# Kernel tuning notes

Hardware: AMD Instinct MI355X
Metric: run time of the kernel (lower is better)

## Reference

```python
import jax, jax.numpy as jnp
import numpy as np

K_INIT = 16  # self.k from __init__

def setup_inputs() -> dict:
    key = jax.random.key(0)
    center = jax.random.normal(key, (8192, 64), dtype=jnp.float32)
    return {"center": center}

def _cdist(x):
    # Euclidean pairwise distances, matmul-based like torch.cdist(p=2).
    x2 = jnp.sum(x * x, axis=-1)  # [N]
    d2 = x2[:, None] + x2[None, :] - 2.0 * (x @ x.T)  # [N, N]
    d2 = jnp.maximum(d2, 0.0)
    # safe sqrt (grad-safe at 0; forward identical)
    d = jnp.sqrt(jnp.where(d2 > 0.0, d2, 1.0))
    return jnp.where(d2 > 0.0, d, 0.0)

def reference(center):
    n, d_feat = center.shape
    k = min(K_INIT + 1, d_feat)  # faithful to torch: min(self.k + 1, center.shape[1])
    dist = _cdist(center)  # [N, N]
    # smallest-k via top_k on negated distances
    _, indices = jax.lax.top_k(-dist, k)  # [N, k]
    neighbor_indices = indices[:, 1:]  # drop self, [N, k-1]
    mean_dists = jnp.take_along_axis(dist, neighbor_indices, axis=1).mean(axis=1)  # [N]
    logp = jax.nn.log_softmax(mean_dists, axis=0)  # = softmax(mean_dists).log()
    q = 1.0 / n
    # F.kl_div(p.log(), q, reduction='sum') = sum q * (log q - log p)
    loss = jnp.sum(q * (jnp.log(jnp.float32(q)) - logp))
    return loss
```

## Files before the change

### kernel.cpp

```cpp
#include <hip/hip_runtime.h>
#include <hip/hip_bf16.h>
#include <math.h>

#define N_PTS 8192
#define D_FEAT 64
#define TPB 1024
#define ROWS_B 32
#define PASSES 16
#define RSTR 648
#define LSTR 20

typedef __attribute__((ext_vector_type(8))) short short8v;
typedef __attribute__((ext_vector_type(16))) float f32x16;

__device__ ushort g_X2[N_PTS * D_FEAT];
__device__ float  g_x2n[N_PTS];
__device__ float  g_md[N_PTS];

__global__ __launch_bounds__(256) void pack_kernel(const float* __restrict__ x) {
    const int gt = blockIdx.x * 256 + threadIdx.x;
    const int row = gt >> 1, half = gt & 1;
    const int chunk = row >> 5, r = row & 31;
    const float4* xr = (const float4*)(x + (size_t)row * D_FEAT + half * 32);
    ushort* base = g_X2 + (size_t)chunk * 2048 + r * 8;
    float norm = 0.f;
    #pragma unroll
    for (int it = 0; it < 4; ++it) {
        float4 a = xr[2 * it], b = xr[2 * it + 1];
        float vals[8] = {a.x, a.y, a.z, a.w, b.x, b.y, b.z, b.w};
        uint hi[8];
        #pragma unroll
        for (int e = 0; e < 8; ++e) {
            float v = vals[e];
            norm += v * v;
            uint u = __float_as_uint(v);
            hi[e] = (u + 0x7fffu + ((u >> 16) & 1u)) >> 16;
        }
        *(uint4*)(base + (half * 4 + it) * 256) = make_uint4(
            hi[0] | (hi[1] << 16), hi[2] | (hi[3] << 16),
            hi[4] | (hi[5] << 16), hi[6] | (hi[7] << 16));
    }
    norm += __shfl_xor(norm, 1);
    if (half == 0) g_x2n[row] = norm;
}

#define CE(A, B) { float lo_, hi_; \
    asm("v_min_f32 %0, %2, %3\n\tv_max_f32 %1, %2, %3" \
        : "=&v"(lo_), "=&v"(hi_) : "v"(A), "v"(B)); \
    A = lo_; B = hi_; }
#define VMIN(D, A, B) { float r_; \
    asm("v_min_f32 %0, %1, %2" : "=v"(r_) : "v"(A), "v"(B)); D = r_; }

__global__ __launch_bounds__(TPB, 4) void nn_kernel() {
    __shared__ float s_mem[32 * RSTR];
    const int t    = threadIdx.x;
    const int lane = t & 63;
    const int w    = t >> 6;
    const int il   = lane & 31;
    const int h    = lane >> 5;
    const int ib   = blockIdx.x;
    const int i0   = ib * ROWS_B;
    const float INF = __builtin_inff();

    {
        float4* s4 = (float4*)s_mem;
        const float4* g4 = (const float4*)g_x2n;
        #pragma unroll
        for (int q = 0; q < 2; ++q) s4[t + q * TPB] = g4[t + q * TPB];
    }

    const short8v* Xf = (const short8v*)g_X2;

    short8v bfr[4];
    {
        const short8v* bp = Xf + ((size_t)ib * 8 + h) * 32 + il;
        #pragma unroll
        for (int tt = 0; tt < 4; ++tt) bfr[tt] = bp[tt * 64];
    }
    __syncthreads();

    float t16[16];
    #pragma unroll
    for (int k = 0; k < 16; ++k) t16[k] = INF;

    const short8v* abase = Xf + ((size_t)w * 8 + h) * 32 + il;
    #define ALOAD(dst, p) { \
        const short8v* ab_ = abase + (size_t)(p) * 4096; \
        _Pragma("unroll") \
        for (int tt = 0; tt < 4; ++tt) dst[tt] = ab_[tt * 64]; }

    #define EPILOG(accv, p) { \
        const int cl_ = (p) * 16 + w; \
        float c[16]; \
        _Pragma("unroll") \
        for (int g = 0; g < 4; ++g) { \
            float4 xq = *(const float4*)&s_mem[cl_ * 32 + 8 * g + 4 * h]; \
            float cand[4] = {xq.x, xq.y, xq.z, xq.w}; \
            _Pragma("unroll") \
            for (int e = 0; e < 4; ++e) \
                c[4 * g + e] = fmaf(-2.f, accv[4 * g + e], cand[e]); \
        } \
         \
        CE(c[0],c[8]) CE(c[1],c[9]) CE(c[2],c[10]) CE(c[3],c[11]) \
        CE(c[4],c[12]) CE(c[5],c[13]) CE(c[6],c[14]) CE(c[7],c[15]) \
        CE(c[0],c[4]) CE(c[1],c[5]) CE(c[2],c[6]) CE(c[3],c[7]) \
        CE(c[8],c[12]) CE(c[9],c[13]) CE(c[10],c[14]) CE(c[11],c[15]) \
        CE(c[4],c[8]) CE(c[5],c[9]) CE(c[6],c[10]) CE(c[7],c[11]) \
        CE(c[0],c[2]) CE(c[1],c[3]) CE(c[4],c[6]) CE(c[5],c[7]) \
        CE(c[8],c[10]) CE(c[9],c[11]) CE(c[12],c[14]) CE(c[13],c[15]) \
        CE(c[2],c[8]) CE(c[3],c[9]) CE(c[6],c[12]) CE(c[7],c[13]) \
        CE(c[2],c[4]) CE(c[3],c[5]) CE(c[6],c[8]) CE(c[7],c[9]) \
        CE(c[10],c[12]) CE(c[11],c[13]) \
        CE(c[0],c[1]) CE(c[2],c[3]) CE(c[4],c[5]) CE(c[6],c[7]) \
        CE(c[8],c[9]) CE(c[10],c[11]) CE(c[12],c[13]) CE(c[14],c[15]) \
        CE(c[1],c[8]) CE(c[3],c[10]) CE(c[5],c[12]) CE(c[7],c[14]) \
        CE(c[1],c[4]) CE(c[3],c[6]) CE(c[5],c[8]) CE(c[7],c[10]) \
        CE(c[9],c[12]) CE(c[11],c[14]) \
        CE(c[1],c[2]) CE(c[3],c[4]) CE(c[5],c[6]) CE(c[7],c[8]) \
        CE(c[9],c[10]) CE(c[11],c[12]) CE(c[13],c[14]) \
         \
        _Pragma("unroll") \
        for (int i = 0; i < 16; ++i) VMIN(t16[i], t16[i], c[15 - i]) \
        _Pragma("unroll") \
        for (int j = 8; j > 0; j >>= 1) { \
            _Pragma("unroll") \
            for (int i = 0; i < 16; ++i) { \
                const int ix = i ^ j; \
                if (ix > i) { CE(t16[i], t16[ix]) } \
            } \
        } }

    #define MFMA4(accv, areg) { \
        _Pragma("unroll") \
        for (int r = 0; r < 16; ++r) accv[r] = 0.f; \
        _Pragma("unroll") \
        for (int tt = 0; tt < 4; ++tt) \
            accv = __builtin_amdgcn_mfma_f32_32x32x16_bf16(areg[tt], bfr[tt], accv, 0, 0, 0); }

    short8v a0[4], a1[4];
    f32x16 acc;
    ALOAD(a0, 0);
    #pragma unroll 1
    for (int pp = 0; pp < PASSES / 2; ++pp) {
        const int p0 = 2 * pp, p1 = 2 * pp + 1;
        ALOAD(a1, p1);
        MFMA4(acc, a0);
        EPILOG(acc, p0);
        if (pp < PASSES / 2 - 1) ALOAD(a0, p0 + 2);
        MFMA4(acc, a1);
        EPILOG(acc, p1);
    }

    {
        const bool own = (w == (ib & 15)) && (h == ((il >> 2) & 1));
        if (own) {
            #pragma unroll
            for (int k = 0; k < 15; ++k) t16[k] = t16[k + 1];
            t16[15] = INF;
        }
    }

    __syncthreads();
    {
        const int list = w * 2 + h;
        float* dst = &s_mem[il * RSTR + list * LSTR];
        *(float4*)(dst + 0)  = make_float4(t16[0],  t16[1],  t16[2],  t16[3]);
        *(float4*)(dst + 4)  = make_float4(t16[4],  t16[5],  t16[6],  t16[7]);
        *(float4*)(dst + 8)  = make_float4(t16[8],  t16[9],  t16[10], t16[11]);
        *(float4*)(dst + 12) = make_float4(t16[12], t16[13], t16[14], t16[15]);
    }
    __syncthreads();

    {
        const int q  = lane >> 5;
        const int sl = lane & 31;
        const int r  = w * 2 + q;
        const int row = i0 + r;
        float tl[16];
        {
            const float* src = &s_mem[r * RSTR + sl * LSTR];
            float4 q0 = *(const float4*)(src + 0);
            float4 q1 = *(const float4*)(src + 4);
            float4 q2 = *(const float4*)(src + 8);
            float4 q3 = *(const float4*)(src + 12);
            tl[0]=q0.x; tl[1]=q0.y; tl[2]=q0.z; tl[3]=q0.w;
            tl[4]=q1.x; tl[5]=q1.y; tl[6]=q1.z; tl[7]=q1.w;
            tl[8]=q2.x; tl[9]=q2.y; tl[10]=q2.z; tl[11]=q2.w;
            tl[12]=q3.x; tl[13]=q3.y; tl[14]=q3.z; tl[15]=q3.w;
        }
        const float x2r = g_x2n[row];
        float sum = 0.f;
        #pragma unroll 1
        for (int it = 0; it < 16; ++it) {
            float m = tl[0]; int src = sl;
            #pragma unroll
            for (int off = 16; off > 0; off >>= 1) {
                float om = __shfl_xor(m, off);
                int os = __shfl_xor(src, off);
                if (om < m || (om == m && os < src)) { m = om; src = os; }
            }
            sum += sqrtf(fmaxf(m + x2r, 0.f));
            const bool pop = (sl == src);
            #pragma unroll
            for (int k = 0; k < 15; ++k) tl[k] = pop ? tl[k + 1] : tl[k];
            tl[15] = pop ? INF : tl[15];
        }
        if (sl == 0) g_md[row] = sum * (1.f / 16.f);
    }
}

__global__ __launch_bounds__(1024) void loss_kernel(float* __restrict__ out) {
    __shared__ float s[1024];
    const int t = threadIdx.x;

    float m = -__builtin_inff();
    for (int j = t; j < N_PTS; j += 1024) m = fmaxf(m, g_md[j]);
    s[t] = m; __syncthreads();
    for (int off = 512; off > 0; off >>= 1) {
        if (t < off) s[t] = fmaxf(s[t], s[t + off]);
        __syncthreads();
    }
    m = s[0]; __syncthreads();

    float se = 0.f, sm = 0.f;
    for (int j = t; j < N_PTS; j += 1024) {
        float v = g_md[j];
        se += expf(v - m);
        sm += v;
    }
    s[t] = se; __syncthreads();
    for (int off = 512; off > 0; off >>= 1) {
        if (t < off) s[t] += s[t + off];
        __syncthreads();
    }
    float S = s[0]; __syncthreads();
    s[t] = sm; __syncthreads();
    for (int off = 512; off > 0; off >>= 1) {
        if (t < off) s[t] += s[t + off];
        __syncthreads();
    }
    float M = s[0];

    if (t == 0) {
        const float n = (float)N_PTS;
        out[0] = -logf(n) - M / n + (m + logf(S));
    }
}

extern "C" void kernel_launch(void* const* d_in, const int* in_sizes, int n_in,
                              void* d_out, int out_size, void* d_ws, size_t ws_size,
                              hipStream_t stream) {
    const float* x = (const float*)d_in[0];
    float* out = (float*)d_out;

    pack_kernel<<<N_PTS * 2 / 256, 256, 0, stream>>>(x);
    nn_kernel<<<N_PTS / ROWS_B, TPB, 0, stream>>>();
    loss_kernel<<<1, 1024, 0, stream>>>(out);
}
```

Measured before the change: 57.99 us.

## Split candidate range across two blocks per row tile and merge partial top-16

Each 32-row tile is now processed by two 512-thread blocks, each scanning half of the candidate points. Each block writes its sorted top-16 partial distances to a global buffer. A new merge kernel combines the two lists per row, then takes sqrt and the mean. This doubles the grid and halves the block size to raise occupancy and parallelism, at the cost of an extra kernel launch and a global round trip for the partial lists.

```diff
diff --git a/kernel.cpp b/kernel.cpp
--- a/kernel.cpp
+++ b/kernel.cpp
@@ -4,17 +4,20 @@
 
 #define N_PTS 8192
 #define D_FEAT 64
-#define TPB 1024
+#define TPB 512
 #define ROWS_B 32
-#define PASSES 16
-#define RSTR 648
-#define LSTR 20
+#define JSPLIT 2
+#define JRANGE (N_PTS / JSPLIT)
+#define CHUNKS_PB (JRANGE / 32)
+#define PASSES (CHUNKS_PB / 8)
+#define LSTRIDE 260
 
 typedef __attribute__((ext_vector_type(8))) short short8v;
 typedef __attribute__((ext_vector_type(16))) float f32x16;
 
 __device__ ushort g_X2[N_PTS * D_FEAT];
 __device__ float  g_x2n[N_PTS];
+__device__ float  g_part[N_PTS * 32];
 __device__ float  g_md[N_PTS];
 
 __global__ __launch_bounds__(256) void pack_kernel(const float* __restrict__ x) {
@@ -52,19 +55,21 @@
     asm("v_min_f32 %0, %1, %2" : "=v"(r_) : "v"(A), "v"(B)); D = r_; }
 
 __global__ __launch_bounds__(TPB, 4) void nn_kernel() {
-    __shared__ float s_mem[32 * RSTR];
+    __shared__ float s_mem[32 * LSTRIDE];
     const int t    = threadIdx.x;
     const int lane = t & 63;
     const int w    = t >> 6;
     const int il   = lane & 31;
     const int h    = lane >> 5;
-    const int ib   = blockIdx.x;
+    const int ib   = blockIdx.x >> 1;
+    const int js   = blockIdx.x & 1;
     const int i0   = ib * ROWS_B;
+    const int c0   = js * CHUNKS_PB;
     const float INF = __builtin_inff();
 
     {
         float4* s4 = (float4*)s_mem;
-        const float4* g4 = (const float4*)g_x2n;
+        const float4* g4 = (const float4*)(g_x2n + js * JRANGE);
         #pragma unroll
         for (int q = 0; q < 2; ++q) s4[t + q * TPB] = g4[t + q * TPB];
     }
@@ -83,14 +88,14 @@
     #pragma unroll
     for (int k = 0; k < 16; ++k) t16[k] = INF;
 
-    const short8v* abase = Xf + ((size_t)w * 8 + h) * 32 + il;
+    const short8v* abase = Xf + ((size_t)(c0 + w) * 8 + h) * 32 + il;
     #define ALOAD(dst, p) { \
-        const short8v* ab_ = abase + (size_t)(p) * 4096; \
+        const short8v* ab_ = abase + (size_t)(p) * 2048; \
         _Pragma("unroll") \
         for (int tt = 0; tt < 4; ++tt) dst[tt] = ab_[tt * 64]; }
 
     #define EPILOG(accv, p) { \
-        const int cl_ = (p) * 16 + w; \
+        const int cl_ = (p) * 8 + w; \
         float c[16]; \
         _Pragma("unroll") \
         for (int g = 0; g < 4; ++g) { \
@@ -152,7 +157,8 @@
     }
 
     {
-        const bool own = (w == (ib & 15)) && (h == ((il >> 2) & 1));
+        const bool own = ((ib >> 7) == js) && (w == (ib & 7)) &&
+                         (h == ((il >> 2) & 1));
         if (own) {
             #pragma unroll
             for (int k = 0; k < 15; ++k) t16[k] = t16[k + 1];
@@ -163,7 +169,7 @@
     __syncthreads();
     {
         const int list = w * 2 + h;
-        float* dst = &s_mem[il * RSTR + list * LSTR];
+        float* dst = &s_mem[il * LSTRIDE + list * 16];
         *(float4*)(dst + 0)  = make_float4(t16[0],  t16[1],  t16[2],  t16[3]);
         *(float4*)(dst + 4)  = make_float4(t16[4],  t16[5],  t16[6],  t16[7]);
         *(float4*)(dst + 8)  = make_float4(t16[8],  t16[9],  t16[10], t16[11]);
@@ -172,13 +178,13 @@
     __syncthreads();
 
     {
-        const int q  = lane >> 5;
-        const int sl = lane & 31;
-        const int r  = w * 2 + q;
+        const int q  = lane >> 4;
+        const int sl = lane & 15;
+        const int r  = w * 4 + q;
         const int row = i0 + r;
         float tl[16];
         {
-            const float* src = &s_mem[r * RSTR + sl * LSTR];
+            const float* src = &s_mem[r * LSTRIDE + sl * 16];
             float4 q0 = *(const float4*)(src + 0);
             float4 q1 = *(const float4*)(src + 4);
             float4 q2 = *(const float4*)(src + 8);
@@ -188,25 +194,44 @@
             tl[8]=q2.x; tl[9]=q2.y; tl[10]=q2.z; tl[11]=q2.w;
             tl[12]=q3.x; tl[13]=q3.y; tl[14]=q3.z; tl[15]=q3.w;
         }
-        const float x2r = g_x2n[row];
-        float sum = 0.f;
         #pragma unroll 1
         for (int it = 0; it < 16; ++it) {
             float m = tl[0]; int src = sl;
             #pragma unroll
-            for (int off = 16; off > 0; off >>= 1) {
+            for (int off = 8; off > 0; off >>= 1) {
                 float om = __shfl_xor(m, off);
                 int os = __shfl_xor(src, off);
                 if (om < m || (om == m && os < src)) { m = om; src = os; }
             }
-            sum += sqrtf(fmaxf(m + x2r, 0.f));
+            if (sl == it) g_part[row * 32 + js * 16 + it] = m;
             const bool pop = (sl == src);
             #pragma unroll
             for (int k = 0; k < 15; ++k) tl[k] = pop ? tl[k + 1] : tl[k];
             tl[15] = pop ? INF : tl[15];
         }
-        if (sl == 0) g_md[row] = sum * (1.f / 16.f);
-    }
+    }
+}
+
+__global__ __launch_bounds__(512) void merge2_kernel() {
+    const int t = threadIdx.x, lane = t & 63, w = t >> 6;
+    const int row = blockIdx.x * 8 + w;
+    const float INF = __builtin_inff();
+    float v = (lane < 32) ? g_part[row * 32 + lane] : INF;
+    const float x2r = g_x2n[row];
+    float sum = 0.f;
+    #pragma unroll 1
+    for (int it = 0; it < 16; ++it) {
+        float m = v; int src = lane;
+        #pragma unroll
+        for (int off = 32; off > 0; off >>= 1) {
+            float om = __shfl_xor(m, off);
+            int os = __shfl_xor(src, off);
+            if (om < m || (om == m && os < src)) { m = om; src = os; }
+        }
+        sum += sqrtf(fmaxf(m + x2r, 0.f));
+        if (lane == src) v = INF;
+    }
+    if (lane == 0) g_md[row] = sum * (1.f / 16.f);
 }
 
 __global__ __launch_bounds__(1024) void loss_kernel(float* __restrict__ out) {
@@ -254,6 +279,7 @@
     float* out = (float*)d_out;
 
     pack_kernel<<<N_PTS * 2 / 256, 256, 0, stream>>>(x);
-    nn_kernel<<<N_PTS / ROWS_B, TPB, 0, stream>>>();
+    nn_kernel<<<(N_PTS / ROWS_B) * JSPLIT, TPB, 0, stream>>>();
+    merge2_kernel<<<N_PTS / 8, 512, 0, stream>>>();
     loss_kernel<<<1, 1024, 0, stream>>>(out);
 }
```

Result: slower. 78.32 us (+35.1%).
